# Kernel tuning notes

Hardware: AMD Instinct MI355X
Metric: run time of the kernel (lower is better)

## Reference

```python
import jax, jax.numpy as jnp
import numpy as np

NEG_INF = -1e9  # finite stand-in for torch's masked_fill(-inf); grad-safe


def setup_inputs() -> dict:
    key = jax.random.key(0)
    k1, k2, k3, k4, k5 = jax.random.split(key, 5)
    B, T, S, Dq, Dk = 8, 2048, 4096, 128, 128
    query = jax.random.normal(k1, (B, T, Dq), dtype=jnp.float32)
    memory_bank = jax.random.normal(k2, (B, S, Dk), dtype=jnp.float32)
    # lengths in [1, S] so every row has at least one valid source position
    memory_lengths = jax.random.randint(k3, (B,), 1, S + 1, dtype=jnp.int64)
    # nn.Linear weights: linear_in [Dk, Dq], linear_out [Dq, Dq+Dk]
    W_in = jax.random.normal(k4, (Dk, Dq), dtype=jnp.float32) / np.sqrt(Dq)
    W_out = jax.random.normal(k5, (Dq, Dq + Dk), dtype=jnp.float32) / np.sqrt(Dq + Dk)
    return {"query": query, "memory_bank": memory_bank,
            "memory_lengths": memory_lengths, "W_in": W_in, "W_out": W_out}


def reference(query, memory_bank, memory_lengths, W_in, W_out):
    B, T, Dq = query.shape
    S = memory_bank.shape[1]
    # score: project query then bmm with sources -> [B, T, S]
    h_t = jnp.einsum('btq,kq->btk', query, W_in)
    align = jnp.einsum('btk,bsk->bts', h_t, memory_bank)
    # mask invalid source positions
    valid = jnp.arange(S) < memory_lengths[:, None]            # [B, S]
    align = jnp.where(valid[:, None, :], align, NEG_INF)       # [B, T, S]
    align_vectors = jax.nn.softmax(align, axis=-1)
    # context and output projection
    c = jnp.einsum('bts,bsk->btk', align_vectors, memory_bank)  # [B, T, Dk]
    concat_c = jnp.concatenate([c, query], axis=-1)             # [B, T, Dk+Dq]
    attn_h = jnp.tanh(jnp.einsum('btc,qc->btq', concat_c, W_out))
    return attn_h, align_vectors, align
```

## Files before the change

### kernel.cpp

```cpp
#include <hip/hip_runtime.h>

#define B_ 8
#define T_ 2048
#define S_ 4096
#define D_ 128
#define N_ (B_*T_)
#define NTILE_ (S_/128)
#define NEG_INF_ (-1e9f)

typedef __attribute__((ext_vector_type(8))) short bf16x8;
typedef __attribute__((ext_vector_type(4))) float f32x4;

__device__ __forceinline__ int load_len(const int* __restrict__ p, int b) {
    return (p[1] == 0) ? p[2*b] : p[b];
}

__device__ __forceinline__ unsigned short f2bf(float x) {
    unsigned u = __float_as_uint(x);
    unsigned r = (u + 0x7fffu + ((u >> 16) & 1u)) >> 16;
    return (unsigned short)r;
}
__device__ __forceinline__ float bf2f(unsigned short h) {
    return __uint_as_float(((unsigned)h) << 16);
}
__device__ __forceinline__ unsigned pk2(unsigned short a, unsigned short b) {
    return (unsigned)a | ((unsigned)b << 16);
}

__global__ __launch_bounds__(256) void prep_mb(
    const float* __restrict__ mb,
    unsigned short* __restrict__ mbh, unsigned short* __restrict__ mbl,
    unsigned short* __restrict__ mbth, unsigned short* __restrict__ mbtl)
{
    __shared__ float tile[64][65];
    const int b = blockIdx.z, f0 = blockIdx.y << 6, s0 = blockIdx.x << 6;
    const int t = threadIdx.x;
#pragma unroll
    for (int i = 0; i < 4; ++i) {
        const int c = t + (i << 8);
        const int s = c >> 4, q = c & 15;
        const long long ga = ((long long)(b*S_ + s0 + s)) * 128 + f0 + q*4;
        const float4 v = *(const float4*)&mb[ga];
        tile[s][q*4+0] = v.x; tile[s][q*4+1] = v.y;
        tile[s][q*4+2] = v.z; tile[s][q*4+3] = v.w;
        unsigned short h0=f2bf(v.x), h1=f2bf(v.y), h2=f2bf(v.z), h3=f2bf(v.w);
        uint2 ph; ph.x = pk2(h0,h1); ph.y = pk2(h2,h3);
        *(uint2*)&mbh[ga] = ph;
        uint2 pl; pl.x = pk2(f2bf(v.x - bf2f(h0)), f2bf(v.y - bf2f(h1)));
        pl.y = pk2(f2bf(v.z - bf2f(h2)), f2bf(v.w - bf2f(h3)));
        *(uint2*)&mbl[ga] = pl;
    }
    __syncthreads();
    const int f = t >> 2, q = t & 3;
    unsigned short h[16], l[16];
#pragma unroll
    for (int ss = 0; ss < 16; ++ss) {
        const float v = tile[q*16 + ss][f];
        h[ss] = f2bf(v);
        l[ss] = f2bf(v - bf2f(h[ss]));
    }
    const long long go = ((long long)(b*128 + f0 + f)) * S_ + s0 + q*16;
    uint4 w0, w1;
    w0.x=pk2(h[0],h[1]);  w0.y=pk2(h[2],h[3]);  w0.z=pk2(h[4],h[5]);  w0.w=pk2(h[6],h[7]);
    w1.x=pk2(h[8],h[9]);  w1.y=pk2(h[10],h[11]);w1.z=pk2(h[12],h[13]);w1.w=pk2(h[14],h[15]);
    *(uint4*)&mbth[go] = w0; *(uint4*)&mbth[go+8] = w1;
    w0.x=pk2(l[0],l[1]);  w0.y=pk2(l[2],l[3]);  w0.z=pk2(l[4],l[5]);  w0.w=pk2(l[6],l[7]);
    w1.x=pk2(l[8],l[9]);  w1.y=pk2(l[10],l[11]);w1.z=pk2(l[12],l[13]);w1.w=pk2(l[14],l[15]);
    *(uint4*)&mbtl[go] = w0; *(uint4*)&mbtl[go+8] = w1;
}

__global__ __launch_bounds__(256) void ht_gemm(
    const float* __restrict__ A, const float* __restrict__ Bmat,
    float* __restrict__ C)
{
    __shared__ float At[16][128];
    __shared__ float Bt[16][128];
    const int t  = threadIdx.x;
    const int tx = t & 15, ty = t >> 4;
    const int n0 = blockIdx.y << 7;
    const int r_ld = t >> 1, kf = t & 1;

    float acc[8][8];
#pragma unroll
    for (int i = 0; i < 8; ++i)
#pragma unroll
        for (int j = 0; j < 8; ++j) acc[i][j] = 0.f;

    const float* Arow = &A[(long long)(n0 + r_ld) * 128];
    const float* Brow = &Bmat[(long long)r_ld * 128];

    for (int k0 = 0; k0 < 128; k0 += 16) {
        __syncthreads();
#pragma unroll
        for (int u = 0; u < 2; ++u) {
            const int kk = kf*8 + u*4;
            const float4 va = *(const float4*)&Arow[k0 + kk];
            At[kk+0][r_ld] = va.x; At[kk+1][r_ld] = va.y;
            At[kk+2][r_ld] = va.z; At[kk+3][r_ld] = va.w;
            const float4 vb = *(const float4*)&Brow[k0 + kk];
            Bt[kk+0][r_ld] = vb.x; Bt[kk+1][r_ld] = vb.y;
            Bt[kk+2][r_ld] = vb.z; Bt[kk+3][r_ld] = vb.w;
        }
        __syncthreads();
#pragma unroll
        for (int kk = 0; kk < 16; ++kk) {
            float a[8], bv[8];
#pragma unroll
            for (int u = 0; u < 2; ++u) {
                const float4 v = *(const float4*)&At[kk][ty*8 + u*4];
                a[u*4+0]=v.x; a[u*4+1]=v.y; a[u*4+2]=v.z; a[u*4+3]=v.w;
                const float4 w = *(const float4*)&Bt[kk][tx*4 + u*64];
                bv[u*4+0]=w.x; bv[u*4+1]=w.y; bv[u*4+2]=w.z; bv[u*4+3]=w.w;
            }
#pragma unroll
            for (int i = 0; i < 8; ++i)
#pragma unroll
                for (int j = 0; j < 8; ++j)
                    acc[i][j] = fmaf(a[i], bv[j], acc[i][j]);
        }
    }
#pragma unroll
    for (int i = 0; i < 8; ++i) {
        float* Crow = &C[(long long)(n0 + ty*8 + i) * 128];
        float4 w0, w1;
        w0.x=acc[i][0]; w0.y=acc[i][1]; w0.z=acc[i][2]; w0.w=acc[i][3];
        w1.x=acc[i][4]; w1.y=acc[i][5]; w1.z=acc[i][6]; w1.w=acc[i][7];
        *(float4*)&Crow[tx*4]      = w0;
        *(float4*)&Crow[tx*4 + 64] = w1;
    }
}

__global__ __launch_bounds__(256) void split_bf16(
    const float* __restrict__ in, unsigned short* __restrict__ hi,
    unsigned short* __restrict__ lo, int n4)
{
    const int i = blockIdx.x * 256 + threadIdx.x;
    if (i >= n4) return;
    const float4 v = *(const float4*)&in[i*4];
    unsigned short h0=f2bf(v.x), h1=f2bf(v.y), h2=f2bf(v.z), h3=f2bf(v.w);
    uint2 ph; ph.x = pk2(h0,h1); ph.y = pk2(h2,h3);
    *(uint2*)&hi[i*4] = ph;
    uint2 pl; pl.x = pk2(f2bf(v.x-bf2f(h0)), f2bf(v.y-bf2f(h1)));
    pl.y = pk2(f2bf(v.z-bf2f(h2)), f2bf(v.w-bf2f(h3)));
    *(uint2*)&lo[i*4] = pl;
}

__global__ __launch_bounds__(256) void qk_mfma(
    const unsigned short* __restrict__ hth, const unsigned short* __restrict__ htl,
    const unsigned short* __restrict__ mbh, const unsigned short* __restrict__ mbl,
    float* __restrict__ alignO, const int* __restrict__ mlen,
    float* __restrict__ pmax, float* __restrict__ psum)
{
    __shared__ __align__(16) unsigned short Ah[128*40], Al[128*40];
    __shared__ __align__(16) unsigned short Bh[128*40], Bl[128*40];
    __shared__ float sm[2][128], ss[2][128];
    const int t = threadIdx.x, l = t & 63, w = t >> 6;
    const int wm = w >> 1, wn = w & 1, g = l >> 4, lr = l & 15;
    const int c0 = blockIdx.x << 7, n0 = blockIdx.y << 7;
    const int b  = blockIdx.y >> 4;
    const int len = load_len(mlen, b);

    if (c0 >= len) {
        const int r = t >> 1, half = (t & 1) << 6;
        float4 neg; neg.x = neg.y = neg.z = neg.w = NEG_INF_;
        float* Crow = &alignO[(long long)(n0 + r) * S_ + c0 + half];
#pragma unroll
        for (int q = 0; q < 16; ++q) *(float4*)&Crow[q*4] = neg;
        if (t < 128) {
            pmax[(long long)blockIdx.x * N_ + n0 + t] = NEG_INF_;
            psum[(long long)blockIdx.x * N_ + n0 + t] = 128.f;
        }
        return;
    }

    f32x4 acc[4][4];
#pragma unroll
    for (int mt = 0; mt < 4; ++mt)
#pragma unroll
        for (int nt = 0; nt < 4; ++nt) acc[mt][nt] = (f32x4)0.f;

    for (int k0 = 0; k0 < 128; k0 += 32) {
        __syncthreads();
#pragma unroll
        for (int i = 0; i < 2; ++i) {
            const int c = t + (i << 8);
            const int row = c >> 2, sl = c & 3;
            const int go = (n0 + row)*128 + k0 + sl*8;
            *(uint4*)&Ah[row*40 + sl*8] = *(const uint4*)&hth[go];
            *(uint4*)&Al[row*40 + sl*8] = *(const uint4*)&htl[go];
            const long long gb = ((long long)b*S_ + c0 + row)*128 + k0 + sl*8;
            *(uint4*)&Bh[row*40 + sl*8] = *(const uint4*)&mbh[gb];
            *(uint4*)&Bl[row*40 + sl*8] = *(const uint4*)&mbl[gb];
        }
        __syncthreads();
        bf16x8 ah[4], al[4];
#pragma unroll
        for (int mt = 0; mt < 4; ++mt) {
            const int r = wm*64 + mt*16 + lr;
            ah[mt] = *(const bf16x8*)&Ah[r*40 + g*8];
            al[mt] = *(const bf16x8*)&Al[r*40 + g*8];
        }
#pragma unroll
        for (int nt = 0; nt < 4; ++nt) {
            const int cc = wn*64 + nt*16 + lr;
            const bf16x8 bh = *(const bf16x8*)&Bh[cc*40 + g*8];
            const bf16x8 bl = *(const bf16x8*)&Bl[cc*40 + g*8];
#pragma unroll
            for (int mt = 0; mt < 4; ++mt) {
                acc[mt][nt] = __builtin_amdgcn_mfma_f32_16x16x32_bf16(ah[mt], bh, acc[mt][nt], 0, 0, 0);
                acc[mt][nt] = __builtin_amdgcn_mfma_f32_16x16x32_bf16(ah[mt], bl, acc[mt][nt], 0, 0, 0);
                acc[mt][nt] = __builtin_amdgcn_mfma_f32_16x16x32_bf16(al[mt], bh, acc[mt][nt], 0, 0, 0);
            }
        }
    }

#pragma unroll
    for (int nt = 0; nt < 4; ++nt) {
        const int col = c0 + wn*64 + nt*16 + lr;
        if (col >= len) {
#pragma unroll
            for (int mt = 0; mt < 4; ++mt)
#pragma unroll
                for (int j = 0; j < 4; ++j) acc[mt][nt][j] = NEG_INF_;
        }
    }
#pragma unroll
    for (int mt = 0; mt < 4; ++mt) {
        float m[4] = {-3.4e38f, -3.4e38f, -3.4e38f, -3.4e38f};
#pragma unroll
        for (int nt = 0; nt < 4; ++nt)
#pragma unroll
            for (int j = 0; j < 4; ++j) m[j] = fmaxf(m[j], acc[mt][nt][j]);
#pragma unroll
        for (int j = 0; j < 4; ++j)
#pragma unroll
            for (int off = 1; off < 16; off <<= 1)
                m[j] = fmaxf(m[j], __shfl_xor(m[j], off, 64));
        float s[4] = {0.f, 0.f, 0.f, 0.f};
#pragma unroll
        for (int nt = 0; nt < 4; ++nt)
#pragma unroll
            for (int j = 0; j < 4; ++j) s[j] += __expf(acc[mt][nt][j] - m[j]);
#pragma unroll
        for (int j = 0; j < 4; ++j)
#pragma unroll
            for (int off = 1; off < 16; off <<= 1)
                s[j] += __shfl_xor(s[j], off, 64);
        if (lr == 0) {
#pragma unroll
            for (int j = 0; j < 4; ++j) {
                const int row = wm*64 + mt*16 + 4*g + j;
                sm[wn][row] = m[j]; ss[wn][row] = s[j];
            }
        }
#pragma unroll
        for (int nt = 0; nt < 4; ++nt) {
            const int col = c0 + wn*64 + nt*16 + lr;
#pragma unroll
            for (int j = 0; j < 4; ++j)
                alignO[(long long)(n0 + wm*64 + mt*16 + 4*g + j)*S_ + col] = acc[mt][nt][j];
        }
    }
    __syncthreads();
    if (t < 128) {
        const float m0 = sm[0][t], m1 = sm[1][t];
        const float M = fmaxf(m0, m1);
        const float Sv = ss[0][t]*__expf(m0 - M) + ss[1][t]*__expf(m1 - M);
        pmax[(long long)blockIdx.x * N_ + n0 + t] = M;
        psum[(long long)blockIdx.x * N_ + n0 + t] = Sv;
    }
}

__global__ __launch_bounds__(256) void merge_stats(
    const float* __restrict__ pmax, const float* __restrict__ psum,
    float* __restrict__ rmax, float* __restrict__ rrinv)
{
    const int r = blockIdx.x * 256 + threadIdx.x;
    float pm[NTILE_];
    float M = -3.4e38f;
#pragma unroll
    for (int i = 0; i < NTILE_; ++i) {
        pm[i] = pmax[(long long)i * N_ + r];
        M = fmaxf(M, pm[i]);
    }
    float S = 0.f;
#pragma unroll
    for (int i = 0; i < NTILE_; ++i)
        S += psum[(long long)i * N_ + r] * __expf(pm[i] - M);
    rmax[r]  = M;
    rrinv[r] = 1.0f / S;
}

__global__ __launch_bounds__(256) void pv_mfma(
    const float* __restrict__ alignI,
    const unsigned short* __restrict__ mbth, const unsigned short* __restrict__ mbtl,
    const float* __restrict__ rmax, const float* __restrict__ rrinv,
    const int* __restrict__ mlen,
    float* __restrict__ av, float* __restrict__ cpart, const int sChunks)
{
    __shared__ __align__(16) unsigned short Ph[128*40], Pl[128*40];
    __shared__ __align__(16) unsigned short Vh[128*40], Vl[128*40];
    const int t = threadIdx.x, l = t & 63, w = t >> 6;
    const int wm = w >> 1, wn = w & 1, g = l >> 4, lr = l & 15;
    const int n0 = blockIdx.y << 7, b = blockIdx.y >> 4;
    const int r_st = t >> 1, hf = t & 1;
    const int len = load_len(mlen, b);
    const float M = rmax[n0 + r_st], R = rrinv[n0 + r_st];

    f32x4 acc[4][4];
#pragma unroll
    for (int mt = 0; mt < 4; ++mt)
#pragma unroll
        for (int nt = 0; nt < 4; ++nt) acc[mt][nt] = (f32x4)0.f;

    const int s00 = blockIdx.x * sChunks * 32;
    for (int ch = 0; ch < sChunks; ++ch) {
        const int s0 = s00 + (ch << 5);
        if (s0 >= len) {
            const long long ga = (long long)(n0 + r_st)*S_ + s0 + hf*16;
            float4 z; z.x = z.y = z.z = z.w = 0.f;
#pragma unroll
            for (int q = 0; q < 4; ++q) *(float4*)&av[ga + q*4] = z;
            continue;
        }
        __syncthreads();
        {
            unsigned short ph[16], pl[16];
            const long long ga = (long long)(n0 + r_st)*S_ + s0 + hf*16;
#pragma unroll
            for (int q = 0; q < 4; ++q) {
                const float4 v = *(const float4*)&alignI[ga + q*4];
                float4 p;
                p.x = __expf(v.x - M)*R; p.y = __expf(v.y - M)*R;
                p.z = __expf(v.z - M)*R; p.w = __expf(v.w - M)*R;
                *(float4*)&av[ga + q*4] = p;
                ph[q*4+0]=f2bf(p.x); pl[q*4+0]=f2bf(p.x - bf2f(ph[q*4+0]));
                ph[q*4+1]=f2bf(p.y); pl[q*4+1]=f2bf(p.y - bf2f(ph[q*4+1]));
                ph[q*4+2]=f2bf(p.z); pl[q*4+2]=f2bf(p.z - bf2f(ph[q*4+2]));
                ph[q*4+3]=f2bf(p.w); pl[q*4+3]=f2bf(p.w - bf2f(ph[q*4+3]));
            }
            uint4 w0, w1;
            w0.x=pk2(ph[0],ph[1]);  w0.y=pk2(ph[2],ph[3]);  w0.z=pk2(ph[4],ph[5]);  w0.w=pk2(ph[6],ph[7]);
            w1.x=pk2(ph[8],ph[9]);  w1.y=pk2(ph[10],ph[11]);w1.z=pk2(ph[12],ph[13]);w1.w=pk2(ph[14],ph[15]);
            *(uint4*)&Ph[r_st*40 + hf*16]     = w0;
            *(uint4*)&Ph[r_st*40 + hf*16 + 8] = w1;
            w0.x=pk2(pl[0],pl[1]);  w0.y=pk2(pl[2],pl[3]);  w0.z=pk2(pl[4],pl[5]);  w0.w=pk2(pl[6],pl[7]);
            w1.x=pk2(pl[8],pl[9]);  w1.y=pk2(pl[10],pl[11]);w1.z=pk2(pl[12],pl[13]);w1.w=pk2(pl[14],pl[15]);
            *(uint4*)&Pl[r_st*40 + hf*16]     = w0;
            *(uint4*)&Pl[r_st*40 + hf*16 + 8] = w1;
        }
#pragma unroll
        for (int i = 0; i < 2; ++i) {
            const int c = t + (i << 8);
            const int f = c >> 2, sl = c & 3;
            const long long gv = ((long long)(b*128 + f))*S_ + s0 + sl*8;
            *(uint4*)&Vh[f*40 + sl*8] = *(const uint4*)&mbth[gv];
            *(uint4*)&Vl[f*40 + sl*8] = *(const uint4*)&mbtl[gv];
        }
        __syncthreads();
        bf16x8 ph[4], pl[4];
#pragma unroll
        for (int mt = 0; mt < 4; ++mt) {
            const int r = wm*64 + mt*16 + lr;
            ph[mt] = *(const bf16x8*)&Ph[r*40 + g*8];
            pl[mt] = *(const bf16x8*)&Pl[r*40 + g*8];
        }
#pragma unroll
        for (int nt = 0; nt < 4; ++nt) {
            const int f = wn*64 + nt*16 + lr;
            const bf16x8 vh = *(const bf16x8*)&Vh[f*40 + g*8];
            const bf16x8 vl = *(const bf16x8*)&Vl[f*40 + g*8];
#pragma unroll
            for (int mt = 0; mt < 4; ++mt) {
                acc[mt][nt] = __builtin_amdgcn_mfma_f32_16x16x32_bf16(ph[mt], vh, acc[mt][nt], 0, 0, 0);
                acc[mt][nt] = __builtin_amdgcn_mfma_f32_16x16x32_bf16(ph[mt], vl, acc[mt][nt], 0, 0, 0);
                acc[mt][nt] = __builtin_amdgcn_mfma_f32_16x16x32_bf16(pl[mt], vh, acc[mt][nt], 0, 0, 0);
            }
        }
    }

    float* cp = cpart + (long long)blockIdx.x * N_ * 128;
#pragma unroll
    for (int mt = 0; mt < 4; ++mt)
#pragma unroll
        for (int nt = 0; nt < 4; ++nt)
#pragma unroll
            for (int j = 0; j < 4; ++j)
                cp[(long long)(n0 + wm*64 + mt*16 + 4*g + j)*128 + wn*64 + nt*16 + lr]
                    = acc[mt][nt][j];
}

__global__ __launch_bounds__(256) void combine_proj(
    const float* __restrict__ cpart, const int nSplit,
    const float* __restrict__ query, const float* __restrict__ Wout,
    float* __restrict__ attn)
{
    __shared__ float Cl[32][132];
    __shared__ float Ql[32][132];
    const int n0 = blockIdx.x << 5;
    const int t = threadIdx.x;
    const int r = t >> 3, kq = t & 7;
#pragma unroll
    for (int f = 0; f < 4; ++f) {
        const int k = kq*16 + f*4;
        const long long idx = (long long)(n0 + r) * 128 + k;
        float4 s4 = *(const float4*)&cpart[idx];
        for (int p = 1; p < nSplit; ++p) {
            const float4 v = *(const float4*)&cpart[(long long)p * N_ * 128 + idx];
            s4.x += v.x; s4.y += v.y; s4.z += v.z; s4.w += v.w;
        }
        *(float4*)&Cl[r][k] = s4;
        *(float4*)&Ql[r][k] = *(const float4*)&query[idx];
    }
    __syncthreads();

    const int j = t & 127, rh = t >> 7;
    float acc2[16];
#pragma unroll
    for (int rr = 0; rr < 16; ++rr) acc2[rr] = 0.f;
    const float4* Wrow = (const float4*)&Wout[j * 256];

    for (int k4 = 0; k4 < 32; ++k4) {
        const float4 w = Wrow[k4];
#pragma unroll
        for (int rr = 0; rr < 16; ++rr) {
            const float4 c4 = *(const float4*)&Cl[rh*16 + rr][k4*4];
            acc2[rr] = fmaf(c4.x, w.x, fmaf(c4.y, w.y, fmaf(c4.z, w.z, fmaf(c4.w, w.w, acc2[rr]))));
        }
    }
    for (int k4 = 0; k4 < 32; ++k4) {
        const float4 w = Wrow[32 + k4];
#pragma unroll
        for (int rr = 0; rr < 16; ++rr) {
            const float4 q4 = *(const float4*)&Ql[rh*16 + rr][k4*4];
            acc2[rr] = fmaf(q4.x, w.x, fmaf(q4.y, w.y, fmaf(q4.z, w.z, fmaf(q4.w, w.w, acc2[rr]))));
        }
    }
#pragma unroll
    for (int rr = 0; rr < 16; ++rr)
        attn[(long long)(n0 + rh*16 + rr) * 128 + j] = tanhf(acc2[rr]);
}

extern "C" void kernel_launch(void* const* d_in, const int* in_sizes, int n_in,
                              void* d_out, int out_size, void* d_ws, size_t ws_size,
                              hipStream_t stream)
{
    const float* query = (const float*)d_in[0];
    const float* mb    = (const float*)d_in[1];
    const int*   mlen  = (const int*)d_in[2];
    const float* Win   = (const float*)d_in[3];
    const float* Wout  = (const float*)d_in[4];

    float* attn  = (float*)d_out;
    float* av    = attn + (size_t)N_ * D_;
    float* align = av   + (size_t)N_ * S_;

    char* p = (char*)d_ws;
    float* rmax  = (float*)p;                 p += (size_t)N_ * 4;
    float* rrinv = (float*)p;                 p += (size_t)N_ * 4;
    float* pmax  = (float*)p;                 p += (size_t)NTILE_ * N_ * 4;
    float* psum  = (float*)p;                 p += (size_t)NTILE_ * N_ * 4;
    float* ht    = (float*)p;                 p += (size_t)N_ * D_ * 4;
    unsigned short* hth  = (unsigned short*)p; p += (size_t)N_ * D_ * 2;
    unsigned short* htl  = (unsigned short*)p; p += (size_t)N_ * D_ * 2;
    unsigned short* mbh  = (unsigned short*)p; p += (size_t)B_ * S_ * D_ * 2;
    unsigned short* mbl  = (unsigned short*)p; p += (size_t)B_ * S_ * D_ * 2;
    unsigned short* mbth = (unsigned short*)p; p += (size_t)B_ * S_ * D_ * 2;
    unsigned short* mbtl = (unsigned short*)p; p += (size_t)B_ * S_ * D_ * 2;
    const size_t usedBase = (size_t)(p - (char*)d_ws);
    const size_t matB = (size_t)N_ * D_ * 4;

    int split;
    float* cpart;
    if (ws_size >= usedBase + 4*matB)      { split = 4; cpart = (float*)p; }
    else if (ws_size >= usedBase + 2*matB) { split = 2; cpart = (float*)p; }
    else if (ws_size >= usedBase + matB)   { split = 1; cpart = (float*)p; }
    else                                   { split = 1; cpart = attn; }

    prep_mb<<<dim3(S_/64, 2, B_), 256, 0, stream>>>(mb, mbh, mbl, mbth, mbtl);
    ht_gemm<<<dim3(1, N_/128), 256, 0, stream>>>(query, Win, ht);
    split_bf16<<<(N_*D_/4)/256, 256, 0, stream>>>(ht, hth, htl, N_*D_/4);
    qk_mfma<<<dim3(S_/128, N_/128), 256, 0, stream>>>(
        hth, htl, mbh, mbl, align, mlen, pmax, psum);
    merge_stats<<<N_/256, 256, 0, stream>>>(pmax, psum, rmax, rrinv);
    pv_mfma<<<dim3(split, N_/128), 256, 0, stream>>>(
        align, mbth, mbtl, rmax, rrinv, mlen, av, cpart, (S_/32)/split);
    combine_proj<<<N_/32, 256, 0, stream>>>(cpart, split, query, Wout, attn);
}
```

Before: 808.6 us.

## Use single bf16 for PV matmul, raise S-split to 8, coalesce mask fill

The PV product drops the three-term split-bf16 emulation (hi*hi + hi*lo + lo*hi) and uses only the high bf16 parts of probabilities and transposed memory, so MFMA work, LDS traffic and the low-part transposed buffer all go away. The S dimension split for pv_mfma can now go up to 8 when the workspace allows it, which raises parallelism at the cost of more partial-sum traffic in combine_proj. The masked-tile fill in qk_mfma is reordered so that consecutive threads write contiguous addresses. The context output loses precision because it now uses plain bf16, and this may exceed fp32 tolerance.

```diff
diff --git a/kernel.cpp b/kernel.cpp
--- a/kernel.cpp
+++ b/kernel.cpp
@@ -30,7 +30,7 @@
 __global__ __launch_bounds__(256) void prep_mb(
     const float* __restrict__ mb,
     unsigned short* __restrict__ mbh, unsigned short* __restrict__ mbl,
-    unsigned short* __restrict__ mbth, unsigned short* __restrict__ mbtl)
+    unsigned short* __restrict__ mbth)
 {
     __shared__ float tile[64][65];
     const int b = blockIdx.z, f0 = blockIdx.y << 6, s0 = blockIdx.x << 6;
@@ -52,21 +52,14 @@
     }
     __syncthreads();
     const int f = t >> 2, q = t & 3;
-    unsigned short h[16], l[16];
-#pragma unroll
-    for (int ss = 0; ss < 16; ++ss) {
-        const float v = tile[q*16 + ss][f];
-        h[ss] = f2bf(v);
-        l[ss] = f2bf(v - bf2f(h[ss]));
-    }
+    unsigned short h[16];
+#pragma unroll
+    for (int ss = 0; ss < 16; ++ss) h[ss] = f2bf(tile[q*16 + ss][f]);
     const long long go = ((long long)(b*128 + f0 + f)) * S_ + s0 + q*16;
     uint4 w0, w1;
     w0.x=pk2(h[0],h[1]);  w0.y=pk2(h[2],h[3]);  w0.z=pk2(h[4],h[5]);  w0.w=pk2(h[6],h[7]);
     w1.x=pk2(h[8],h[9]);  w1.y=pk2(h[10],h[11]);w1.z=pk2(h[12],h[13]);w1.w=pk2(h[14],h[15]);
     *(uint4*)&mbth[go] = w0; *(uint4*)&mbth[go+8] = w1;
-    w0.x=pk2(l[0],l[1]);  w0.y=pk2(l[2],l[3]);  w0.z=pk2(l[4],l[5]);  w0.w=pk2(l[6],l[7]);
-    w1.x=pk2(l[8],l[9]);  w1.y=pk2(l[10],l[11]);w1.z=pk2(l[12],l[13]);w1.w=pk2(l[14],l[15]);
-    *(uint4*)&mbtl[go] = w0; *(uint4*)&mbtl[go+8] = w1;
 }
 
 __global__ __launch_bounds__(256) void ht_gemm(
@@ -161,11 +154,13 @@
     const int len = load_len(mlen, b);
 
     if (c0 >= len) {
-        const int r = t >> 1, half = (t & 1) << 6;
         float4 neg; neg.x = neg.y = neg.z = neg.w = NEG_INF_;
-        float* Crow = &alignO[(long long)(n0 + r) * S_ + c0 + half];
-#pragma unroll
-        for (int q = 0; q < 16; ++q) *(float4*)&Crow[q*4] = neg;
+#pragma unroll
+        for (int i = 0; i < 16; ++i) {
+            const int c = i*1024 + t*4;
+            const int row = c >> 7, col = c & 127;
+            *(float4*)&alignO[(long long)(n0 + row)*S_ + c0 + col] = neg;
+        }
         if (t < 128) {
             pmax[(long long)blockIdx.x * N_ + n0 + t] = NEG_INF_;
             psum[(long long)blockIdx.x * N_ + n0 + t] = 128.f;
@@ -293,13 +288,13 @@
 
 __global__ __launch_bounds__(256) void pv_mfma(
     const float* __restrict__ alignI,
-    const unsigned short* __restrict__ mbth, const unsigned short* __restrict__ mbtl,
+    const unsigned short* __restrict__ mbth,
     const float* __restrict__ rmax, const float* __restrict__ rrinv,
     const int* __restrict__ mlen,
     float* __restrict__ av, float* __restrict__ cpart, const int sChunks)
 {
-    __shared__ __align__(16) unsigned short Ph[128*40], Pl[128*40];
-    __shared__ __align__(16) unsigned short Vh[128*40], Vl[128*40];
+    __shared__ __align__(16) unsigned short Ph[128*40];
+    __shared__ __align__(16) unsigned short Vh[128*40];
     const int t = threadIdx.x, l = t & 63, w = t >> 6;
     const int wm = w >> 1, wn = w & 1, g = l >> 4, lr = l & 15;
     const int n0 = blockIdx.y << 7, b = blockIdx.y >> 4;
@@ -325,7 +320,7 @@
         }
         __syncthreads();
         {
-            unsigned short ph[16], pl[16];
+            unsigned short ph[16];
             const long long ga = (long long)(n0 + r_st)*S_ + s0 + hf*16;
 #pragma unroll
             for (int q = 0; q < 4; ++q) {
@@ -334,20 +329,14 @@
                 p.x = __expf(v.x - M)*R; p.y = __expf(v.y - M)*R;
                 p.z = __expf(v.z - M)*R; p.w = __expf(v.w - M)*R;
                 *(float4*)&av[ga + q*4] = p;
-                ph[q*4+0]=f2bf(p.x); pl[q*4+0]=f2bf(p.x - bf2f(ph[q*4+0]));
-                ph[q*4+1]=f2bf(p.y); pl[q*4+1]=f2bf(p.y - bf2f(ph[q*4+1]));
-                ph[q*4+2]=f2bf(p.z); pl[q*4+2]=f2bf(p.z - bf2f(ph[q*4+2]));
-                ph[q*4+3]=f2bf(p.w); pl[q*4+3]=f2bf(p.w - bf2f(ph[q*4+3]));
+                ph[q*4+0]=f2bf(p.x); ph[q*4+1]=f2bf(p.y);
+                ph[q*4+2]=f2bf(p.z); ph[q*4+3]=f2bf(p.w);
             }
             uint4 w0, w1;
             w0.x=pk2(ph[0],ph[1]);  w0.y=pk2(ph[2],ph[3]);  w0.z=pk2(ph[4],ph[5]);  w0.w=pk2(ph[6],ph[7]);
             w1.x=pk2(ph[8],ph[9]);  w1.y=pk2(ph[10],ph[11]);w1.z=pk2(ph[12],ph[13]);w1.w=pk2(ph[14],ph[15]);
             *(uint4*)&Ph[r_st*40 + hf*16]     = w0;
             *(uint4*)&Ph[r_st*40 + hf*16 + 8] = w1;
-            w0.x=pk2(pl[0],pl[1]);  w0.y=pk2(pl[2],pl[3]);  w0.z=pk2(pl[4],pl[5]);  w0.w=pk2(pl[6],pl[7]);
-            w1.x=pk2(pl[8],pl[9]);  w1.y=pk2(pl[10],pl[11]);w1.z=pk2(pl[12],pl[13]);w1.w=pk2(pl[14],pl[15]);
-            *(uint4*)&Pl[r_st*40 + hf*16]     = w0;
-            *(uint4*)&Pl[r_st*40 + hf*16 + 8] = w1;
         }
 #pragma unroll
         for (int i = 0; i < 2; ++i) {
@@ -355,27 +344,18 @@
             const int f = c >> 2, sl = c & 3;
             const long long gv = ((long long)(b*128 + f))*S_ + s0 + sl*8;
             *(uint4*)&Vh[f*40 + sl*8] = *(const uint4*)&mbth[gv];
-            *(uint4*)&Vl[f*40 + sl*8] = *(const uint4*)&mbtl[gv];
-        }
-        __syncthreads();
-        bf16x8 ph[4], pl[4];
-#pragma unroll
-        for (int mt = 0; mt < 4; ++mt) {
-            const int r = wm*64 + mt*16 + lr;
-            ph[mt] = *(const bf16x8*)&Ph[r*40 + g*8];
-            pl[mt] = *(const bf16x8*)&Pl[r*40 + g*8];
-        }
+        }
+        __syncthreads();
+        bf16x8 ph[4];
+#pragma unroll
+        for (int mt = 0; mt < 4; ++mt)
+            ph[mt] = *(const bf16x8*)&Ph[(wm*64 + mt*16 + lr)*40 + g*8];
 #pragma unroll
         for (int nt = 0; nt < 4; ++nt) {
-            const int f = wn*64 + nt*16 + lr;
-            const bf16x8 vh = *(const bf16x8*)&Vh[f*40 + g*8];
-            const bf16x8 vl = *(const bf16x8*)&Vl[f*40 + g*8];
-#pragma unroll
-            for (int mt = 0; mt < 4; ++mt) {
+            const bf16x8 vh = *(const bf16x8*)&Vh[(wn*64 + nt*16 + lr)*40 + g*8];
+#pragma unroll
+            for (int mt = 0; mt < 4; ++mt)
                 acc[mt][nt] = __builtin_amdgcn_mfma_f32_16x16x32_bf16(ph[mt], vh, acc[mt][nt], 0, 0, 0);
-                acc[mt][nt] = __builtin_amdgcn_mfma_f32_16x16x32_bf16(ph[mt], vl, acc[mt][nt], 0, 0, 0);
-                acc[mt][nt] = __builtin_amdgcn_mfma_f32_16x16x32_bf16(pl[mt], vh, acc[mt][nt], 0, 0, 0);
-            }
         }
     }
 
@@ -466,24 +446,24 @@
     unsigned short* mbh  = (unsigned short*)p; p += (size_t)B_ * S_ * D_ * 2;
     unsigned short* mbl  = (unsigned short*)p; p += (size_t)B_ * S_ * D_ * 2;
     unsigned short* mbth = (unsigned short*)p; p += (size_t)B_ * S_ * D_ * 2;
-    unsigned short* mbtl = (unsigned short*)p; p += (size_t)B_ * S_ * D_ * 2;
     const size_t usedBase = (size_t)(p - (char*)d_ws);
     const size_t matB = (size_t)N_ * D_ * 4;
 
     int split;
     float* cpart;
-    if (ws_size >= usedBase + 4*matB)      { split = 4; cpart = (float*)p; }
+    if (ws_size >= usedBase + 8*matB)      { split = 8; cpart = (float*)p; }
+    else if (ws_size >= usedBase + 4*matB) { split = 4; cpart = (float*)p; }
     else if (ws_size >= usedBase + 2*matB) { split = 2; cpart = (float*)p; }
     else if (ws_size >= usedBase + matB)   { split = 1; cpart = (float*)p; }
     else                                   { split = 1; cpart = attn; }
 
-    prep_mb<<<dim3(S_/64, 2, B_), 256, 0, stream>>>(mb, mbh, mbl, mbth, mbtl);
+    prep_mb<<<dim3(S_/64, 2, B_), 256, 0, stream>>>(mb, mbh, mbl, mbth);
     ht_gemm<<<dim3(1, N_/128), 256, 0, stream>>>(query, Win, ht);
     split_bf16<<<(N_*D_/4)/256, 256, 0, stream>>>(ht, hth, htl, N_*D_/4);
     qk_mfma<<<dim3(S_/128, N_/128), 256, 0, stream>>>(
         hth, htl, mbh, mbl, align, mlen, pmax, psum);
     merge_stats<<<N_/256, 256, 0, stream>>>(pmax, psum, rmax, rrinv);
     pv_mfma<<<dim3(split, N_/128), 256, 0, stream>>>(
-        align, mbth, mbtl, rmax, rrinv, mlen, av, cpart, (S_/32)/split);
+        align, mbth, rmax, rrinv, mlen, av, cpart, (S_/32)/split);
     combine_proj<<<N_/32, 256, 0, stream>>>(cpart, split, query, Wout, attn);
 }
```

After: 794.3 us. About the same (-1.8%).
